# Kernel tuning notes

Hardware: AMD Instinct MI355X
Metric: run time of the kernel (lower is better)

The kernel has to match this reference:

```python
import jax, jax.numpy as jnp
import numpy as np

N = 4_194_304
L = 15
SLOPE = 0.01  # torch LeakyReLU default


def setup_inputs() -> dict:
    key = jax.random.key(0)
    ks = jax.random.split(key, 16)
    n = jax.random.normal
    return {
        "x": n(ks[0], (N, 2), jnp.float32),
        # scale Linear(1,1) per layer (small init keeps exp(log_scale) stable)
        "scale_w": n(ks[1], (L, 1, 1), jnp.float32) * 0.2,
        "scale_b": n(ks[2], (L, 1), jnp.float32) * 0.1,
        # g_theta_scale: 1->32->16->1
        "sW1": n(ks[3], (L, 1, 32), jnp.float32) * 0.5,
        "sb1": n(ks[4], (L, 32), jnp.float32) * 0.1,
        "sW2": n(ks[5], (L, 32, 16), jnp.float32) * 0.2,
        "sb2": n(ks[6], (L, 16), jnp.float32) * 0.1,
        "sW3": n(ks[7], (L, 16, 1), jnp.float32) * 0.2,
        "sb3": n(ks[8], (L, 1), jnp.float32) * 0.1,
        # g_theta_shift: 1->32->16->1
        "tW1": n(ks[9], (L, 1, 32), jnp.float32) * 0.5,
        "tb1": n(ks[10], (L, 32), jnp.float32) * 0.1,
        "tW2": n(ks[11], (L, 32, 16), jnp.float32) * 0.2,
        "tb2": n(ks[12], (L, 16), jnp.float32) * 0.1,
        "tW3": n(ks[13], (L, 16, 1), jnp.float32) * 0.2,
        "tb3": n(ks[14], (L, 1), jnp.float32) * 0.1,
    }


def _mlp(h, W1, b1, W2, b2, W3, b3):
    h = jax.nn.leaky_relu(h @ W1 + b1, SLOPE)
    h = jax.nn.leaky_relu(h @ W2 + b2, SLOPE)
    return h @ W3 + b3


def reference(x, scale_w, scale_b, sW1, sb1, sW2, sb2, sW3, sb3,
              tW1, tb1, tW2, tb2, tW3, tb3):
    def step(carry, p):
        z1, z2, ld = carry
        sw, sb, w1, b1, w2, b2, w3, b3, u1, c1, u2, c2, u3, c3 = p
        x1, x2 = z2, z1  # swap
        log_scale = jnp.tanh(_mlp(x1, w1, b1, w2, b2, w3, b3)) @ sw + sb
        z2n = jnp.exp(log_scale) * x2 + _mlp(x1, u1, c1, u2, c2, u3, c3)
        return (x1, z2n, ld + log_scale), None

    init = (x[:, 1:2], x[:, 0:1], jnp.zeros_like(x[:, :1]))
    params = (scale_w, scale_b, sW1, sb1, sW2, sb2, sW3, sb3,
              tW1, tb1, tW2, tb2, tW3, tb3)
    (z1, z2, ld), _ = jax.lax.scan(step, init, params)
    return jnp.concatenate((z1, z2), axis=1), ld
```

## Files before the change

### kernel.cpp

```cpp
#include <hip/hip_runtime.h>
#include <math.h>

#define SLOPE 0.01f
#define NLAYER 15
#define FINE_CELLS 512
#define COARSE_CELLS 128
#define CELLS 640
#define FINE_NODES 513
#define NODES_PER_NET 642
#define TABLE_FLOAT4 (NLAYER * CELLS)
#define INV_LN2 1.4426950408889634f
#define LN2F 0.6931471805599453f

__device__ __forceinline__ float fast_exp2(float x) {
#if __has_builtin(__builtin_amdgcn_exp2f)
    return __builtin_amdgcn_exp2f(x);
#else
    return __expf(x * LN2F);
#endif
}

__device__ __forceinline__ float mlp_exact(
    float x1,
    const float* __restrict__ W1, const float* __restrict__ b1,
    const float* __restrict__ W2, const float* __restrict__ b2,
    const float* __restrict__ W3, float b3)
{
    float h2[16];
#pragma unroll
    for (int n = 0; n < 16; ++n) h2[n] = b2[n];
#pragma unroll 2
    for (int j = 0; j < 32; ++j) {
        float h = fmaf(W1[j], x1, b1[j]);
        h = fmaxf(h, SLOPE * h);
#pragma unroll
        for (int n = 0; n < 16; ++n) h2[n] = fmaf(h, W2[j * 16 + n], h2[n]);
    }
    float o = b3;
#pragma unroll
    for (int n = 0; n < 16; ++n) {
        float h = fmaxf(h2[n], SLOPE * h2[n]);
        o = fmaf(h, W3[n], o);
    }
    return o;
}

__global__ __launch_bounds__(640) void build_tables(
    const float* __restrict__ scale_w, const float* __restrict__ scale_b,
    const float* __restrict__ sW1, const float* __restrict__ sb1,
    const float* __restrict__ sW2, const float* __restrict__ sb2,
    const float* __restrict__ sW3, const float* __restrict__ sb3,
    const float* __restrict__ tW1, const float* __restrict__ tb1,
    const float* __restrict__ tW2, const float* __restrict__ tb2,
    const float* __restrict__ tW3, const float* __restrict__ tb3,
    float* __restrict__ ws)
{
    const int m = blockIdx.x;
    const int l = m >> 1;
    const int which = m & 1;
    const float* W1 = (which ? tW1 : sW1) + l * 32;
    const float* b1 = (which ? tb1 : sb1) + l * 32;
    const float* W2 = (which ? tW2 : sW2) + l * 512;
    const float* b2 = (which ? tb2 : sb2) + l * 16;
    const float* W3 = (which ? tW3 : sW3) + l * 16;
    const float  b3 = which ? tb3[l] : sb3[l];

    __shared__ float nodes[NODES_PER_NET];

    for (int i = threadIdx.x; i < NODES_PER_NET; i += blockDim.x) {
        const float x = (i < FINE_NODES) ? (-2.0f + (float)i * (1.0f / 128.0f))
                                         : (-32.0f + (float)(i - FINE_NODES) * 0.5f);
        float o = mlp_exact(x, W1, b1, W2, b2, W3, b3);
        nodes[i] = which ? o : fmaf(tanhf(o), scale_w[l], scale_b[l]) * INV_LN2;
    }
    __syncthreads();

    for (int c = threadIdx.x; c < CELLS; c += blockDim.x) {
        int base; float x_lo, invh;
        if (c < FINE_CELLS) { base = c;     x_lo = -2.0f  + (float)c * (1.0f / 128.0f); invh = 128.0f; }
        else                { base = c + 1; x_lo = -32.0f + (float)(c - FINE_CELLS) * 0.5f; invh = 2.0f; }
        float lo = nodes[base], hi = nodes[base + 1];
        float slope = (hi - lo) * invh;
        float icpt  = fmaf(-slope, x_lo, lo);
        *(float2*)(ws + ((size_t)(l * CELLS + c) * 4) + which * 2) = make_float2(slope, icpt);
    }
}

__device__ __forceinline__ int cell_index(float x) {
    float uf = fmaf(x, 128.0f, 256.0f);
    float uc = fmaf(x, 2.0f, 576.0f);
    float ucl = fminf(fmaxf(uc, 512.0f), 639.0f);
    float u = (fabsf(x) < 2.0f) ? uf : ucl;
    return (int)u;
}

__global__ __launch_bounds__(1024) void flow_lut(
    const float4* __restrict__ x,
    const float4* __restrict__ ws,
    float4* __restrict__ out_z,
    float2* __restrict__ out_ld,
    int npair)
{
    __shared__ __align__(16) float4 lds[TABLE_FLOAT4];
    for (int i = threadIdx.x; i < TABLE_FLOAT4; i += blockDim.x) lds[i] = ws[i];
    __syncthreads();

    const int tid = blockIdx.x * blockDim.x + threadIdx.x;
    const int stride = gridDim.x * blockDim.x;

    for (int p0 = tid; p0 < npair; p0 += 2 * stride) {
        const int p1 = p0 + stride;
        const bool has1 = (p1 < npair);
        float4 xa = x[p0];
        float4 xb = has1 ? x[p1] : make_float4(0.f, 0.f, 0.f, 0.f);

        float az1 = xa.y, az2 = xa.x, ald = 0.f;
        float bz1 = xa.w, bz2 = xa.z, bld = 0.f;
        float cz1 = xb.y, cz2 = xb.x, cld = 0.f;
        float dz1 = xb.w, dz2 = xb.z, dld = 0.f;

#pragma unroll
        for (int l = 0; l < NLAYER; ++l) {
            const float4* T = lds + l * CELLS;
            int ia = cell_index(az2);
            int ib = cell_index(bz2);
            int ic = cell_index(cz2);
            int id = cell_index(dz2);
            float4 ca = T[ia];
            float4 cb = T[ib];
            float4 cc = T[ic];
            float4 cd = T[id];

            float als = fmaf(ca.x, az2, ca.y);
            float ag  = fmaf(ca.z, az2, ca.w);
            float bls = fmaf(cb.x, bz2, cb.y);
            float bg  = fmaf(cb.z, bz2, cb.w);
            float cls = fmaf(cc.x, cz2, cc.y);
            float cg  = fmaf(cc.z, cz2, cc.w);
            float dls = fmaf(cd.x, dz2, cd.y);
            float dg  = fmaf(cd.z, dz2, cd.w);

            float az2n = fmaf(fast_exp2(als), az1, ag);
            float bz2n = fmaf(fast_exp2(bls), bz1, bg);
            float cz2n = fmaf(fast_exp2(cls), cz1, cg);
            float dz2n = fmaf(fast_exp2(dls), dz1, dg);

            az1 = az2; az2 = az2n; ald += als;
            bz1 = bz2; bz2 = bz2n; bld += bls;
            cz1 = cz2; cz2 = cz2n; cld += cls;
            dz1 = dz2; dz2 = dz2n; dld += dls;
        }

        out_z[p0]  = make_float4(az1, az2, bz1, bz2);
        out_ld[p0] = make_float2(ald * LN2F, bld * LN2F);
        if (has1) {
            out_z[p1]  = make_float4(cz1, cz2, dz1, dz2);
            out_ld[p1] = make_float2(cld * LN2F, dld * LN2F);
        }
    }
}

extern "C" void kernel_launch(void* const* d_in, const int* in_sizes, int n_in,
                              void* d_out, int out_size, void* d_ws, size_t ws_size,
                              hipStream_t stream) {
    const int n = in_sizes[0] / 2;
    const int npair = n / 2;

    const float4* x       = (const float4*)d_in[0];
    const float*  scale_w = (const float*)d_in[1];
    const float*  scale_b = (const float*)d_in[2];
    const float*  sW1     = (const float*)d_in[3];
    const float*  sb1     = (const float*)d_in[4];
    const float*  sW2     = (const float*)d_in[5];
    const float*  sb2     = (const float*)d_in[6];
    const float*  sW3     = (const float*)d_in[7];
    const float*  sb3     = (const float*)d_in[8];
    const float*  tW1     = (const float*)d_in[9];
    const float*  tb1     = (const float*)d_in[10];
    const float*  tW2     = (const float*)d_in[11];
    const float*  tb2     = (const float*)d_in[12];
    const float*  tW3     = (const float*)d_in[13];
    const float*  tb3     = (const float*)d_in[14];

    float4* out_z  = (float4*)d_out;
    float2* out_ld = (float2*)((float*)d_out + (size_t)2 * n);

    build_tables<<<30, 640, 0, stream>>>(scale_w, scale_b,
        sW1, sb1, sW2, sb2, sW3, sb3,
        tW1, tb1, tW2, tb2, tW3, tb3, (float*)d_ws);

    flow_lut<<<256, 1024, 0, stream>>>(x, (const float4*)d_ws, out_z, out_ld, npair);
}
```

Before: 147.0 us.

## Store LUT as fp16 slope/midpoint pairs to halve LDS footprint and double occupancy

```diff
diff --git a/kernel.cpp b/kernel.cpp
--- a/kernel.cpp
+++ b/kernel.cpp
@@ -1,4 +1,5 @@
 #include <hip/hip_runtime.h>
+#include <hip/hip_fp16.h>
 #include <math.h>
 
 #define SLOPE 0.01f
@@ -8,7 +9,7 @@
 #define CELLS 640
 #define FINE_NODES 513
 #define NODES_PER_NET 642
-#define TABLE_FLOAT4 (NLAYER * CELLS)
+#define TABLE_CELLS (NLAYER * CELLS)
 #define INV_LN2 1.4426950408889634f
 #define LN2F 0.6931471805599453f
 
@@ -76,33 +77,43 @@
     __syncthreads();
 
     for (int c = threadIdx.x; c < CELLS; c += blockDim.x) {
-        int base; float x_lo, invh;
-        if (c < FINE_CELLS) { base = c;     x_lo = -2.0f  + (float)c * (1.0f / 128.0f); invh = 128.0f; }
-        else                { base = c + 1; x_lo = -32.0f + (float)(c - FINE_CELLS) * 0.5f; invh = 2.0f; }
+        int base; float invh;
+        if (c < FINE_CELLS) { base = c;     invh = 128.0f; }
+        else                { base = c + 1; invh = 2.0f; }
         float lo = nodes[base], hi = nodes[base + 1];
         float slope = (hi - lo) * invh;
-        float icpt  = fmaf(-slope, x_lo, lo);
-        *(float2*)(ws + ((size_t)(l * CELLS + c) * 4) + which * 2) = make_float2(slope, icpt);
-    }
-}
-
-__device__ __forceinline__ int cell_index(float x) {
+        float vmid  = 0.5f * (lo + hi);
+        __half2 h2 = __floats2half2_rn(slope, vmid);
+        ((__half2*)ws)[(size_t)(l * CELLS + c) * 2 + which] = h2;
+    }
+}
+
+__device__ __forceinline__ void cell_addr(float x, int* idx, float* dx) {
     float uf = fmaf(x, 128.0f, 256.0f);
     float uc = fmaf(x, 2.0f, 576.0f);
+    bool fine = (fabsf(x) < 2.0f);
     float ucl = fminf(fmaxf(uc, 512.0f), 639.0f);
-    float u = (fabsf(x) < 2.0f) ? uf : ucl;
-    return (int)u;
-}
-
-__global__ __launch_bounds__(1024) void flow_lut(
+    float fi = fine ? uf : ucl;
+    int i = (int)fi;
+    float fu = (float)i;
+    float u = fine ? uf : uc;
+    float h = fine ? 0.0078125f : 0.5f;
+    *idx = i;
+    *dx = (u - fu - 0.5f) * h;
+}
+
+__global__ __launch_bounds__(1024, 2) void flow_lut(
     const float4* __restrict__ x,
     const float4* __restrict__ ws,
     float4* __restrict__ out_z,
     float2* __restrict__ out_ld,
     int npair)
 {
-    __shared__ __align__(16) float4 lds[TABLE_FLOAT4];
-    for (int i = threadIdx.x; i < TABLE_FLOAT4; i += blockDim.x) lds[i] = ws[i];
+    __shared__ __align__(16) uint2 lds[TABLE_CELLS];
+    {
+        float4* dst = (float4*)lds;
+        for (int i = threadIdx.x; i < TABLE_CELLS / 2; i += blockDim.x) dst[i] = ws[i];
+    }
     __syncthreads();
 
     const int tid = blockIdx.x * blockDim.x + threadIdx.x;
@@ -121,24 +132,31 @@
 
 #pragma unroll
         for (int l = 0; l < NLAYER; ++l) {
-            const float4* T = lds + l * CELLS;
-            int ia = cell_index(az2);
-            int ib = cell_index(bz2);
-            int ic = cell_index(cz2);
-            int id = cell_index(dz2);
-            float4 ca = T[ia];
-            float4 cb = T[ib];
-            float4 cc = T[ic];
-            float4 cd = T[id];
-
-            float als = fmaf(ca.x, az2, ca.y);
-            float ag  = fmaf(ca.z, az2, ca.w);
-            float bls = fmaf(cb.x, bz2, cb.y);
-            float bg  = fmaf(cb.z, bz2, cb.w);
-            float cls = fmaf(cc.x, cz2, cc.y);
-            float cg  = fmaf(cc.z, cz2, cc.w);
-            float dls = fmaf(cd.x, dz2, cd.y);
-            float dg  = fmaf(cd.z, dz2, cd.w);
+            const uint2* T = lds + l * CELLS;
+            int ia, ib, ic, id;
+            float dxa, dxb, dxc, dxd;
+            cell_addr(az2, &ia, &dxa);
+            cell_addr(bz2, &ib, &dxb);
+            cell_addr(cz2, &ic, &dxc);
+            cell_addr(dz2, &id, &dxd);
+            uint2 ca = T[ia];
+            uint2 cb = T[ib];
+            uint2 cc = T[ic];
+            uint2 cd = T[id];
+
+            __half2 ash = *(const __half2*)&ca.x, ath = *(const __half2*)&ca.y;
+            __half2 bsh = *(const __half2*)&cb.x, bth = *(const __half2*)&cb.y;
+            __half2 csh = *(const __half2*)&cc.x, cth = *(const __half2*)&cc.y;
+            __half2 dsh = *(const __half2*)&cd.x, dth = *(const __half2*)&cd.y;
+
+            float als = fmaf(__low2float(ash), dxa, __high2float(ash));
+            float ag  = fmaf(__low2float(ath), dxa, __high2float(ath));
+            float bls = fmaf(__low2float(bsh), dxb, __high2float(bsh));
+            float bg  = fmaf(__low2float(bth), dxb, __high2float(bth));
+            float cls = fmaf(__low2float(csh), dxc, __high2float(csh));
+            float cg  = fmaf(__low2float(cth), dxc, __high2float(cth));
+            float dls = fmaf(__low2float(dsh), dxd, __high2float(dsh));
+            float dg  = fmaf(__low2float(dth), dxd, __high2float(dth));
 
             float az2n = fmaf(fast_exp2(als), az1, ag);
             float bz2n = fmaf(fast_exp2(bls), bz1, bg);
@@ -189,5 +207,5 @@
         sW1, sb1, sW2, sb2, sW3, sb3,
         tW1, tb1, tW2, tb2, tW3, tb3, (float*)d_ws);
 
-    flow_lut<<<256, 1024, 0, stream>>>(x, (const float4*)d_ws, out_z, out_ld, npair);
-}
+    flow_lut<<<512, 1024, 0, stream>>>(x, (const float4*)d_ws, out_z, out_ld, npair);
+}
```

Result: slower. 154.0 us (+4.8%).
